# Kernel tuning notes

Hardware: AMD Instinct MI355X
Metric: run time of the kernel (lower is better)

## Reference

```python
import jax, jax.numpy as jnp
import numpy as np

N_NODES = 100000
N_EDGES = 1600000
N_GRAPHS = 1024
F = 128
L = 3  # num_gnn_layers
EPS = 1e-5


def _ln(x, g, b):
    mu = jnp.mean(x, axis=-1, keepdims=True)
    v = jnp.mean((x - mu) ** 2, axis=-1, keepdims=True)
    return (x - mu) * jax.lax.rsqrt(v + EPS) * g + b


def setup_inputs() -> dict:
    key = jax.random.key(0)
    ks = jax.random.split(key, 40)
    s = 0.05
    d = {}
    d['x'] = jax.random.normal(ks[0], (N_NODES, F), jnp.float32)
    d['w'] = jax.random.uniform(ks[1], (N_NODES, 1), jnp.float32)
    d['edge_index'] = jax.random.randint(ks[2], (2, N_EDGES), 0, N_NODES)
    d['batch'] = jnp.sort(jax.random.randint(ks[3], (N_NODES,), 0, N_GRAPHS))
    # input linear: (monomer_features+1) -> gc_features
    d['W_in'] = jax.random.normal(ks[4], (F + 1, F), jnp.float32) * s
    d['b_in'] = jnp.zeros((F,), jnp.float32)
    # stacked GCBlock params [L, ...]
    d['sage_Wl'] = jax.random.normal(ks[5], (L, F, F), jnp.float32) * s
    d['sage_bl'] = jnp.zeros((L, F), jnp.float32)
    d['sage_Wr'] = jax.random.normal(ks[6], (L, F, F), jnp.float32) * s
    d['ln1_g'] = jnp.ones((L, F), jnp.float32)
    d['ln1_b'] = jnp.zeros((L, F), jnp.float32)
    d['lin1_W'] = jax.random.normal(ks[7], (L, F, F), jnp.float32) * s
    d['lin1_b'] = jnp.zeros((L, F), jnp.float32)
    d['lin2_W'] = jax.random.normal(ks[8], (L, F, F), jnp.float32) * s
    d['lin2_b'] = jnp.zeros((L, F), jnp.float32)
    d['ln2_g'] = jnp.ones((L, F), jnp.float32)
    d['ln2_b'] = jnp.zeros((L, F), jnp.float32)
    # MeanDiffFeatureBlock: Linear(2F -> F)
    d['mdf_W'] = jax.random.normal(ks[9], (2 * F, F), jnp.float32) * s
    d['mdf_b'] = jnp.zeros((F,), jnp.float32)
    # mean PoolingLayer params
    d['pln1_g'] = jnp.ones((F,), jnp.float32)
    d['pln1_b'] = jnp.zeros((F,), jnp.float32)
    d['plin1_W'] = jax.random.normal(ks[10], (F, F), jnp.float32) * s
    d['plin1_b'] = jnp.zeros((F,), jnp.float32)
    d['plin2_W'] = jax.random.normal(ks[11], (F, F), jnp.float32) * s
    d['plin2_b'] = jnp.zeros((F,), jnp.float32)
    d['pln2_g'] = jnp.ones((F,), jnp.float32)
    d['pln2_b'] = jnp.zeros((F,), jnp.float32)
    return d


def reference(x, w, edge_index, batch, W_in, b_in, sage_Wl, sage_bl, sage_Wr,
              ln1_g, ln1_b, lin1_W, lin1_b, lin2_W, lin2_b, ln2_g, ln2_b,
              mdf_W, mdf_b, pln1_g, pln1_b, plin1_W, plin1_b, plin2_W, plin2_b,
              pln2_g, pln2_b):
    src, dst = edge_index[0], edge_index[1]
    # in-degree for SAGE mean aggregation (clamped so isolated nodes -> 0 agg)
    deg = jax.ops.segment_sum(jnp.ones((N_EDGES,), jnp.float32), dst,
                              num_segments=N_NODES)
    deg = jnp.maximum(deg, 1.0)[:, None]
    # graph sizes for global_mean_pool
    cnt = jax.ops.segment_sum(jnp.ones((N_NODES,), jnp.float32), batch,
                              num_segments=N_GRAPHS)
    cnt = jnp.maximum(cnt, 1.0)[:, None]

    # inilinear on [x, weight-fraction]  (scalers are identity at init)
    h = jnp.concatenate([x, w], axis=-1) @ W_in + b_in  # [N, F]

    def gc_block(h, p):
        Wl, bl, Wr, g1, b1, W1, bb1, W2, bb2, g2, b2 = p
        # SAGEConv: lin_l(mean_j x_j) + lin_r(x_i)
        agg = jax.ops.segment_sum(h[src], dst, num_segments=N_NODES) / deg
        y = agg @ Wl + bl + h @ Wr
        y1 = _ln(y + h, g1, b1)
        y2 = jax.nn.elu(y1 @ W1 + bb1) @ W2 + bb2  # dropout = identity (eval)
        return _ln(y2 + y1, g2, b2), None

    h, _ = jax.lax.scan(gc_block, h,
                        (sage_Wl, sage_bl, sage_Wr, ln1_g, ln1_b,
                         lin1_W, lin1_b, lin2_W, lin2_b, ln2_g, ln2_b))

    # MeanDiffFeatureBlock
    gm = jax.ops.segment_sum(h, batch, num_segments=N_GRAPHS) / cnt  # [B, F]
    h = jnp.concatenate([h, h - gm[batch]], axis=-1) @ mdf_W + mdf_b

    # mean PoolingLayer
    p = jax.ops.segment_sum(h, batch, num_segments=N_GRAPHS) / cnt  # [B, F]
    hh = _ln(p, pln1_g, pln1_b)
    y = jax.nn.elu(hh @ plin1_W + plin1_b) @ plin2_W + plin2_b
    return _ln(y + hh, pln2_g, pln2_b)  # [B, F]
```

## Files before the change

### kernel.cpp

```cpp
#include <hip/hip_runtime.h>
#include <math.h>

#define NN 100000
#define NE 1600000
#define NG 1024
#define FF 128
#define BSH 9
#define NBK ((NN + 511) >> BSH)
#define RB 512
#define BCAP 16384

typedef __attribute__((ext_vector_type(8))) short short8;
typedef __attribute__((ext_vector_type(4))) float f32x4;
typedef __attribute__((ext_vector_type(2))) float f32x2;

__device__ __forceinline__ unsigned short f2b(float f) {
    union { float f; unsigned u; } v; v.f = f;
    unsigned r = (v.u + 0x7FFF + ((v.u >> 16) & 1)) >> 16;
    return (unsigned short)r;
}
__device__ __forceinline__ float us2f(unsigned short u) {
    union { unsigned u; float f; } v; v.u = ((unsigned)u) << 16; return v.f;
}
__device__ __forceinline__ float fast_elu(float v) {
    float e = __builtin_amdgcn_exp2f(v * 1.44269504088896340736f) - 1.0f;
    return v > 0.f ? v : e;
}
__device__ __forceinline__ uint2 pk8(const float* v) {
    unsigned lo = 0, hi = 0;
    lo = (unsigned)__builtin_amdgcn_cvt_pk_fp8_f32(v[0], v[1], (int)lo, false);
    lo = (unsigned)__builtin_amdgcn_cvt_pk_fp8_f32(v[2], v[3], (int)lo, true);
    hi = (unsigned)__builtin_amdgcn_cvt_pk_fp8_f32(v[4], v[5], (int)hi, false);
    hi = (unsigned)__builtin_amdgcn_cvt_pk_fp8_f32(v[6], v[7], (int)hi, true);
    uint2 r; r.x = lo; r.y = hi; return r;
}
#define MFMA(a, b, c) __builtin_amdgcn_mfma_f32_16x16x32_bf16((a), (b), (c), 0, 0, 0)

__global__ __launch_bounds__(256)
void radix_scatter(const int* __restrict__ src, const int* __restrict__ dst,
                   int* __restrict__ bcur, unsigned* __restrict__ pairs, int n) {
    __shared__ int base[NBK];
    __shared__ int cnt[NBK];
    for (int i = threadIdx.x; i < NBK; i += 256) cnt[i] = 0;
    __syncthreads();
    const int per = (n + RB - 1) / RB;
    const int beg = blockIdx.x * per;
    const int end = min(n, beg + per);
    for (int i = beg + threadIdx.x; i < end; i += 256)
        atomicAdd(&cnt[dst[i] >> BSH], 1);
    __syncthreads();
    for (int i = threadIdx.x; i < NBK; i += 256)
        base[i] = cnt[i] ? atomicAdd(&bcur[i], cnt[i]) : 0;
    __syncthreads();
    for (int i = beg + threadIdx.x; i < end; i += 256) {
        int d = dst[i];
        int p = atomicAdd(&base[d >> BSH], 1);
        pairs[p] = ((unsigned)src[i] << BSH) | (unsigned)(d & 511);
    }
}

__global__ __launch_bounds__(512)
void bucket_build(const unsigned* __restrict__ pairs, const int* __restrict__ bcur,
                  int* __restrict__ row_beg, int* __restrict__ row_end,
                  float* __restrict__ inv_deg, int* __restrict__ ssrc) {
    __shared__ int cnt[512];
    __shared__ int curs[512];
    __shared__ int wsum[8];
    const int b = blockIdx.x;
    const int n0 = b << BSH;
    const int t = threadIdx.x;
    const int lane = t & 63, wid = t >> 6;

    cnt[t] = 0;
    __syncthreads();
    const int beg = b * BCAP, end = bcur[b];
    for (int i = beg + t; i < end; i += 512)
        atomicAdd(&cnt[pairs[i] & 511], 1);
    __syncthreads();

    int c = cnt[t];
    int x = c;
    #pragma unroll
    for (int o = 1; o < 64; o <<= 1) {
        int y = __shfl_up(x, o);
        if (lane >= o) x += y;
    }
    if (lane == 63) wsum[wid] = x;
    __syncthreads();
    if (t == 0) {
        int s = 0;
        #pragma unroll
        for (int w2 = 0; w2 < 8; ++w2) { int tv = wsum[w2]; wsum[w2] = s; s += tv; }
    }
    __syncthreads();
    int g0 = beg + wsum[wid] + x - c;
    curs[t] = g0;
    {
        int node = n0 + t;
        if (node < NN) {
            row_beg[node] = g0; row_end[node] = g0 + c;
            inv_deg[node] = 1.0f / (float)(c > 1 ? c : 1);
        }
    }
    __syncthreads();
    for (int i = beg + t; i < end; i += 512) {
        unsigned pr = pairs[i];
        int p = atomicAdd(&curs[pr & 511], 1);
        ssrc[p] = (int)(pr >> BSH) << 7;
    }
}

__global__ __launch_bounds__(256)
void graph_offsets(const int* __restrict__ batch, int* __restrict__ g_off,
                   float* __restrict__ inv_cnt, int* __restrict__ bcur,
                   int* __restrict__ ssrc) {
    int g = blockIdx.x * blockDim.x + threadIdx.x;
    if (g == 0) ssrc[0] = 0;
    if (g < NBK) bcur[g] = g * BCAP;
    if (g > NG) return;
    if (g == NG) { g_off[NG] = NN; return; }
    int lo = 0, hi = NN;
    while (lo < hi) { int mid = (lo + hi) >> 1; if (batch[mid] < g) lo = mid + 1; else hi = mid; }
    int lo2 = lo, hi2 = NN;
    while (lo2 < hi2) { int mid = (lo2 + hi2) >> 1; if (batch[mid] < g + 1) lo2 = mid + 1; else hi2 = mid; }
    g_off[g] = lo;
    int c = lo2 - lo;
    inv_cnt[g] = 1.0f / (float)(c > 1 ? c : 1);
}

struct WTab { const float* a[16]; };
__global__ __launch_bounds__(256)
void prep_weights(WTab tab, unsigned short* __restrict__ dst) {
    int w = blockIdx.x >> 6;
    int idx = ((blockIdx.x & 63) << 8) + threadIdx.x;
    int j = idx & 7, lane = (idx >> 3) & 63, nt = (idx >> 9) & 7, kc = idx >> 12;
    int cb = lane & 15, rq = lane >> 4;
    int k = kc * 32 + rq * 8 + j;
    int n = nt * 16 + cb;
    dst[(size_t)w * 16384 + idx] = f2b(tab.a[w][k * 128 + n]);
}

__global__ __launch_bounds__(256)
void sage_agg(const unsigned char* __restrict__ h8, const int* __restrict__ row_beg,
              const int* __restrict__ row_end, const float* __restrict__ inv_deg,
              const int* __restrict__ ssrc, unsigned short* __restrict__ aggb) {
    const int wid = threadIdx.x >> 6;
    const int lane = threadIdx.x & 63;
    const int n0 = blockIdx.x * 8 + wid * 2;
    const int n1 = n0 + 1;
    const int eg = lane >> 4, j = lane & 15;
    const int jo = j * 8;
    const int beg0 = row_beg[n0], end0 = row_end[n0];
    const int beg1 = row_beg[n1], end1 = row_end[n1];
    f32x2 a0 = {0.f, 0.f}, a1 = {0.f, 0.f}, a2 = {0.f, 0.f}, a3 = {0.f, 0.f};
    f32x2 b0 = {0.f, 0.f}, b1 = {0.f, 0.f}, b2 = {0.f, 0.f}, b3 = {0.f, 0.f};
    int e0 = beg0 + eg, e1 = beg1 + eg;
    const int d0 = end0 - beg0, d1 = end1 - beg1;
    const int nit = ((d0 > d1 ? d0 : d1) + 31) >> 5;
    for (int it = 0; it < nit; ++it, e0 += 32, e1 += 32) {
        uint2 u0[8], u1[8];
        #pragma unroll
        for (int k = 0; k < 8; ++k) {
            int ek = e0 + 4 * k;
            bool ok = ek < end0;
            int idx = ssrc[ok ? ek : 0];
            uint2 uu = *(const uint2*)(h8 + (unsigned)(idx + jo));
            uu.x = ok ? uu.x : 0u;
            uu.y = ok ? uu.y : 0u;
            u0[k] = uu;
        }
        #pragma unroll
        for (int k = 0; k < 8; ++k) {
            int ek = e1 + 4 * k;
            bool ok = ek < end1;
            int idx = ssrc[ok ? ek : 0];
            uint2 uu = *(const uint2*)(h8 + (unsigned)(idx + jo));
            uu.x = ok ? uu.x : 0u;
            uu.y = ok ? uu.y : 0u;
            u1[k] = uu;
        }
        #pragma unroll
        for (int k = 0; k < 8; ++k) {
            a0 += __builtin_amdgcn_cvt_pk_f32_fp8(u0[k].x, false);
            a1 += __builtin_amdgcn_cvt_pk_f32_fp8(u0[k].x, true);
            a2 += __builtin_amdgcn_cvt_pk_f32_fp8(u0[k].y, false);
            a3 += __builtin_amdgcn_cvt_pk_f32_fp8(u0[k].y, true);
            b0 += __builtin_amdgcn_cvt_pk_f32_fp8(u1[k].x, false);
            b1 += __builtin_amdgcn_cvt_pk_f32_fp8(u1[k].x, true);
            b2 += __builtin_amdgcn_cvt_pk_f32_fp8(u1[k].y, false);
            b3 += __builtin_amdgcn_cvt_pk_f32_fp8(u1[k].y, true);
        }
    }
    float af[8] = {a0.x, a0.y, a1.x, a1.y, a2.x, a2.y, a3.x, a3.y};
    float bf[8] = {b0.x, b0.y, b1.x, b1.y, b2.x, b2.y, b3.x, b3.y};
    #pragma unroll
    for (int k = 0; k < 8; ++k) {
        af[k] += __shfl_xor(af[k], 16);
        af[k] += __shfl_xor(af[k], 32);
        bf[k] += __shfl_xor(bf[k], 16);
        bf[k] += __shfl_xor(bf[k], 32);
    }
    if (eg == 0) {
        float id0 = inv_deg[n0];
        float id1 = inv_deg[n1];
        #pragma unroll
        for (int nt = 0; nt < 8; ++nt) {
            aggb[(size_t)n0 * 128 + nt * 16 + j] = f2b(af[nt] * id0);
            aggb[(size_t)n1 * 128 + nt * 16 + j] = f2b(bf[nt] * id1);
        }
    }
}

__global__ __launch_bounds__(256)
void pool_mean_b(const unsigned short* __restrict__ src, const int* __restrict__ g_off,
                 const float* __restrict__ inv_cnt, float* __restrict__ out) {
    __shared__ float red[3][128];
    const int g = blockIdx.x;
    const int t = threadIdx.x;
    const int lane = t & 63, wid = t >> 6;
    const int j = lane & 15, rs = lane >> 4;
    const int beg = g_off[g], end = g_off[g + 1];
    float s[8] = {0.f, 0.f, 0.f, 0.f, 0.f, 0.f, 0.f, 0.f};
    for (int n = beg + rs + wid * 4; n < end; n += 16) {
        short8 v = *(const short8*)&src[(size_t)n * FF + j * 8];
        #pragma unroll
        for (int i = 0; i < 8; ++i) s[i] += us2f((unsigned short)v[i]);
    }
    #pragma unroll
    for (int i = 0; i < 8; ++i) {
        s[i] += __shfl_xor(s[i], 16);
        s[i] += __shfl_xor(s[i], 32);
    }
    if (wid > 0 && rs == 0) {
        #pragma unroll
        for (int i = 0; i < 8; ++i) red[wid - 1][j * 8 + i] = s[i];
    }
    __syncthreads();
    if (wid == 0 && rs == 0) {
        float ic = inv_cnt[g];
        #pragma unroll
        for (int i = 0; i < 8; ++i) {
            float v = s[i] + red[0][j * 8 + i] + red[1][j * 8 + i] + red[2][j * 8 + i];
            out[(size_t)g * FF + j * 8 + i] = v * ic;
        }
    }
}

template<bool AB16, bool R1, int RESM, int ACT, bool LN, bool OF32, bool OB16, bool OB8>
__global__ __launch_bounds__(256)
void gemm_mfma(const void* __restrict__ A_,
               const unsigned short* __restrict__ Wf,
               const float* __restrict__ bias,
               const float* __restrict__ rvec, const float* __restrict__ rrow,
               const float* __restrict__ res,
               const float* __restrict__ lng, const float* __restrict__ lnb,
               float* __restrict__ outf, unsigned short* __restrict__ outb,
               unsigned char* __restrict__ outb8, int M) {
    __shared__ short Al[64 * 136];

    const int t = threadIdx.x;
    const int lane = t & 63, wid = t >> 6;
    const int m0 = blockIdx.x * 64;
    const int cb = lane & 15, rq = lane >> 4;
    const int band = wid * 16;

    if (AB16) {
        const unsigned short* Ab = (const unsigned short*)A_;
        #pragma unroll
        for (int i2 = 0; i2 < 4; ++i2) {
            int i = lane + i2 * 64;
            int row = band + (i >> 4), seg = i & 15;
            int gr = m0 + row; if (gr >= M) gr = M - 1;
            *(uint4*)&Al[row * 136 + seg * 8] = *(const uint4*)&Ab[(size_t)gr * 128 + seg * 8];
        }
    } else {
        const float* Af = (const float*)A_;
        #pragma unroll
        for (int i2 = 0; i2 < 8; ++i2) {
            int i = lane + i2 * 64;
            int row = band + (i >> 5), seg = i & 31;
            int gr = m0 + row; if (gr >= M) gr = M - 1;
            float4 v = *(const float4*)&Af[(size_t)gr * 128 + seg * 4];
            ushort4 o = {f2b(v.x), f2b(v.y), f2b(v.z), f2b(v.w)};
            *(ushort4*)&Al[row * 136 + seg * 4] = o;
        }
    }

    f32x4 acc[8];
    #pragma unroll
    for (int nt = 0; nt < 8; ++nt) acc[nt] = (f32x4){0.f, 0.f, 0.f, 0.f};

    const int aoff_base = (band + cb) * 136 + rq * 8;
    for (int kc = 0; kc < 4; ++kc) {
        short8 a0 = *(const short8*)&Al[aoff_base + kc * 32];
        #pragma unroll
        for (int nt = 0; nt < 8; ++nt) {
            short8 b0 = *(const short8*)&Wf[(size_t)(kc * 8 + nt) * 512 + lane * 8];
            acc[nt] = MFMA(a0, b0, acc[nt]);
        }
    }

    float bs[8], rr[8], lg[8], lb[8];
    #pragma unroll
    for (int nt = 0; nt < 8; ++nt) {
        int col = nt * 16 + cb;
        bs[nt] = bias[col];
        if (R1) rr[nt] = rrow[col];
        if (LN) { lg[nt] = lng[col]; lb[nt] = lnb[col]; }
    }
    #pragma unroll
    for (int reg = 0; reg < 4; ++reg) {
        int m = m0 + band + rq * 4 + reg;
        int mc = m < M ? m : M - 1;
        float v[8];
        #pragma unroll
        for (int nt = 0; nt < 8; ++nt) v[nt] = acc[nt][reg] + bs[nt];
        if (R1) {
            float rv = rvec[mc];
            #pragma unroll
            for (int nt = 0; nt < 8; ++nt) v[nt] += rv * rr[nt];
        }
        if (RESM == 1) {
            #pragma unroll
            for (int nt = 0; nt < 8; ++nt) v[nt] += res[(size_t)mc * 128 + nt * 16 + cb];
        }
        if (ACT == 1) {
            #pragma unroll
            for (int nt = 0; nt < 8; ++nt) v[nt] = fast_elu(v[nt]);
        }
        if (LN) {
            float s1 = 0.f, s2 = 0.f;
            #pragma unroll
            for (int nt = 0; nt < 8; ++nt) { s1 += v[nt]; s2 += v[nt] * v[nt]; }
            #pragma unroll
            for (int o = 8; o >= 1; o >>= 1) { s1 += __shfl_xor(s1, o); s2 += __shfl_xor(s2, o); }
            float mu = s1 * (1.f / 128.f);
            float rs = rsqrtf(s2 * (1.f / 128.f) - mu * mu + 1e-5f);
            #pragma unroll
            for (int nt = 0; nt < 8; ++nt) v[nt] = (v[nt] - mu) * rs * lg[nt] + lb[nt];
        }
        if (m < M) {
            #pragma unroll
            for (int nt = 0; nt < 8; ++nt) {
                size_t o = (size_t)m * 128 + nt * 16 + cb;
                if (OF32) outf[o] = v[nt];
                if (OB16) outb[o] = f2b(v[nt]);
            }
            if (OB8) *(uint2*)&outb8[(size_t)m * 128 + cb * 8] = pk8(v);
        }
    }
}

__global__ __launch_bounds__(256)
void gc_chain(const unsigned short* __restrict__ hin, const unsigned short* __restrict__ aggb,
              unsigned short* __restrict__ hout, unsigned char* __restrict__ h8out,
              const unsigned short* __restrict__ Wl_f, const unsigned short* __restrict__ Wr_f,
              const unsigned short* __restrict__ W1_f, const unsigned short* __restrict__ W2_f,
              const float* __restrict__ bl,
              const float* __restrict__ g1, const float* __restrict__ b1,
              const float* __restrict__ bb1, const float* __restrict__ bb2,
              const float* __restrict__ g2, const float* __restrict__ b2, int M) {
    __shared__ short Hl[64 * 136];
    __shared__ short Gl[64 * 136];

    const int t = threadIdx.x;
    const int lane = t & 63, wid = t >> 6;
    const int m0 = blockIdx.x * 64;
    const int cb = lane & 15, rq = lane >> 4;
    const int band = wid * 16;
    const int aoff_base = (band + cb) * 136 + rq * 8;
    const int boff = lane * 8;

    #pragma unroll
    for (int i2 = 0; i2 < 4; ++i2) {
        int i = lane + i2 * 64;
        int row = band + (i >> 4), seg = i & 15;
        int gr = m0 + row; if (gr >= M) gr = M - 1;
        *(uint4*)&Hl[row * 136 + seg * 8] = *(const uint4*)&hin[(size_t)gr * 128 + seg * 8];
        *(uint4*)&Gl[row * 136 + seg * 8] = *(const uint4*)&aggb[(size_t)gr * 128 + seg * 8];
    }

    f32x4 acc[8];
    #pragma unroll
    for (int nt = 0; nt < 8; ++nt) acc[nt] = (f32x4){0.f, 0.f, 0.f, 0.f};

    for (int kc = 0; kc < 4; ++kc) {
        short8 a0 = *(const short8*)&Gl[aoff_base + kc * 32];
        short8 a1 = *(const short8*)&Hl[aoff_base + kc * 32];
        #pragma unroll
        for (int nt = 0; nt < 8; ++nt) {
            const size_t wo = (size_t)(kc * 8 + nt) * 512 + boff;
            acc[nt] = MFMA(a0, *(const short8*)&Wl_f[wo], acc[nt]);
            acc[nt] = MFMA(a1, *(const short8*)&Wr_f[wo], acc[nt]);
        }
    }

    float y1r[4][8];
    {
        float bs[8], lg[8], lb[8];
        #pragma unroll
        for (int nt = 0; nt < 8; ++nt) {
            int col = nt * 16 + cb;
            bs[nt] = bl[col]; lg[nt] = g1[col]; lb[nt] = b1[col];
        }
        #pragma unroll
        for (int reg = 0; reg < 4; ++reg) {
            int r = band + rq * 4 + reg;
            float v[8];
            float s1 = 0.f, s2 = 0.f;
            #pragma unroll
            for (int nt = 0; nt < 8; ++nt) {
                v[nt] = acc[nt][reg] + bs[nt] + us2f((unsigned short)Hl[r * 136 + nt * 16 + cb]);
                s1 += v[nt]; s2 += v[nt] * v[nt];
            }
            #pragma unroll
            for (int o = 8; o >= 1; o >>= 1) { s1 += __shfl_xor(s1, o); s2 += __shfl_xor(s2, o); }
            float mu = s1 * (1.f / 128.f);
            float rs = rsqrtf(s2 * (1.f / 128.f) - mu * mu + 1e-5f);
            #pragma unroll
            for (int nt = 0; nt < 8; ++nt) {
                float y = (v[nt] - mu) * rs * lg[nt] + lb[nt];
                y1r[reg][nt] = y;
                Hl[r * 136 + nt * 16 + cb] = (short)f2b(y);
            }
        }
    }

    #pragma unroll
    for (int nt = 0; nt < 8; ++nt) acc[nt] = (f32x4){0.f, 0.f, 0.f, 0.f};
    for (int kc = 0; kc < 4; ++kc) {
        short8 a0 = *(const short8*)&Hl[aoff_base + kc * 32];
        #pragma unroll
        for (int nt = 0; nt < 8; ++nt)
            acc[nt] = MFMA(a0, *(const short8*)&W1_f[(size_t)(kc * 8 + nt) * 512 + boff], acc[nt]);
    }
    {
        float bs[8];
        #pragma unroll
        for (int nt = 0; nt < 8; ++nt) bs[nt] = bb1[nt * 16 + cb];
        #pragma unroll
        for (int reg = 0; reg < 4; ++reg) {
            int r = band + rq * 4 + reg;
            #pragma unroll
            for (int nt = 0; nt < 8; ++nt) {
                float v = fast_elu(acc[nt][reg] + bs[nt]);
                Gl[r * 136 + nt * 16 + cb] = (short)f2b(v);
            }
        }
    }

    #pragma unroll
    for (int nt = 0; nt < 8; ++nt) acc[nt] = (f32x4){0.f, 0.f, 0.f, 0.f};
    for (int kc = 0; kc < 4; ++kc) {
        short8 a0 = *(const short8*)&Gl[aoff_base + kc * 32];
        #pragma unroll
        for (int nt = 0; nt < 8; ++nt)
            acc[nt] = MFMA(a0, *(const short8*)&W2_f[(size_t)(kc * 8 + nt) * 512 + boff], acc[nt]);
    }
    {
        float bs[8], lg[8], lb[8];
        #pragma unroll
        for (int nt = 0; nt < 8; ++nt) {
            int col = nt * 16 + cb;
            bs[nt] = bb2[col]; lg[nt] = g2[col]; lb[nt] = b2[col];
        }
        #pragma unroll
        for (int reg = 0; reg < 4; ++reg) {
            int r = band + rq * 4 + reg;
            int m = m0 + r;
            float v[8];
            float s1 = 0.f, s2 = 0.f;
            #pragma unroll
            for (int nt = 0; nt < 8; ++nt) {
                v[nt] = acc[nt][reg] + bs[nt] + y1r[reg][nt];
                s1 += v[nt]; s2 += v[nt] * v[nt];
            }
            #pragma unroll
            for (int o = 8; o >= 1; o >>= 1) { s1 += __shfl_xor(s1, o); s2 += __shfl_xor(s2, o); }
            float mu = s1 * (1.f / 128.f);
            float rs = rsqrtf(s2 * (1.f / 128.f) - mu * mu + 1e-5f);
            if (m < M) {
                float fv[8];
                #pragma unroll
                for (int nt = 0; nt < 8; ++nt) {
                    fv[nt] = (v[nt] - mu) * rs * lg[nt] + lb[nt];
                    hout[(size_t)m * 128 + nt * 16 + cb] = f2b(fv[nt]);
                }
                *(uint2*)&h8out[(size_t)m * 128 + cb * 8] = pk8(fv);
            }
        }
    }
}

__global__ __launch_bounds__(256)
void head_chain(const float* __restrict__ gm,
                const unsigned short* __restrict__ Wa_f,
                const unsigned short* __restrict__ P1_f,
                const unsigned short* __restrict__ P2_f,
                const float* __restrict__ mdfb,
                const float* __restrict__ g1, const float* __restrict__ b1,
                const float* __restrict__ p1b, const float* __restrict__ p2b,
                const float* __restrict__ g2, const float* __restrict__ b2,
                float* __restrict__ outp) {
    __shared__ short Al[64 * 136];

    const int t = threadIdx.x;
    const int lane = t & 63, wid = t >> 6;
    const int m0 = blockIdx.x * 64;
    const int cb = lane & 15, rq = lane >> 4;
    const int band = wid * 16;
    const int aoff_base = (band + cb) * 136 + rq * 8;
    const int boff = lane * 8;

    #pragma unroll
    for (int i2 = 0; i2 < 8; ++i2) {
        int i = lane + i2 * 64;
        int row = band + (i >> 5), seg = i & 31;
        float4 v = *(const float4*)&gm[(size_t)(m0 + row) * 128 + seg * 4];
        ushort4 o = {f2b(v.x), f2b(v.y), f2b(v.z), f2b(v.w)};
        *(ushort4*)&Al[row * 136 + seg * 4] = o;
    }

    f32x4 acc[8];
    #pragma unroll
    for (int nt = 0; nt < 8; ++nt) acc[nt] = (f32x4){0.f, 0.f, 0.f, 0.f};
    for (int kc = 0; kc < 4; ++kc) {
        short8 a0 = *(const short8*)&Al[aoff_base + kc * 32];
        #pragma unroll
        for (int nt = 0; nt < 8; ++nt)
            acc[nt] = MFMA(a0, *(const short8*)&Wa_f[(size_t)(kc * 8 + nt) * 512 + boff], acc[nt]);
    }
    float y1r[4][8];
    {
        float bs[8], lg[8], lb[8];
        #pragma unroll
        for (int nt = 0; nt < 8; ++nt) {
            int col = nt * 16 + cb;
            bs[nt] = mdfb[col]; lg[nt] = g1[col]; lb[nt] = b1[col];
        }
        #pragma unroll
        for (int reg = 0; reg < 4; ++reg) {
            int r = band + rq * 4 + reg;
            float v[8];
            float s1 = 0.f, s2 = 0.f;
            #pragma unroll
            for (int nt = 0; nt < 8; ++nt) {
                v[nt] = acc[nt][reg] + bs[nt];
                s1 += v[nt]; s2 += v[nt] * v[nt];
            }
            #pragma unroll
            for (int o = 8; o >= 1; o >>= 1) { s1 += __shfl_xor(s1, o); s2 += __shfl_xor(s2, o); }
            float mu = s1 * (1.f / 128.f);
            float rs = rsqrtf(s2 * (1.f / 128.f) - mu * mu + 1e-5f);
            #pragma unroll
            for (int nt = 0; nt < 8; ++nt) {
                float y = (v[nt] - mu) * rs * lg[nt] + lb[nt];
                y1r[reg][nt] = y;
                Al[r * 136 + nt * 16 + cb] = (short)f2b(y);
            }
        }
    }

    #pragma unroll
    for (int nt = 0; nt < 8; ++nt) acc[nt] = (f32x4){0.f, 0.f, 0.f, 0.f};
    for (int kc = 0; kc < 4; ++kc) {
        short8 a0 = *(const short8*)&Al[aoff_base + kc * 32];
        #pragma unroll
        for (int nt = 0; nt < 8; ++nt)
            acc[nt] = MFMA(a0, *(const short8*)&P1_f[(size_t)(kc * 8 + nt) * 512 + boff], acc[nt]);
    }
    {
        float bs[8];
        #pragma unroll
        for (int nt = 0; nt < 8; ++nt) bs[nt] = p1b[nt * 16 + cb];
        #pragma unroll
        for (int reg = 0; reg < 4; ++reg) {
            int r = band + rq * 4 + reg;
            #pragma unroll
            for (int nt = 0; nt < 8; ++nt) {
                float v = fast_elu(acc[nt][reg] + bs[nt]);
                Al[r * 136 + nt * 16 + cb] = (short)f2b(v);
            }
        }
    }

    #pragma unroll
    for (int nt = 0; nt < 8; ++nt) acc[nt] = (f32x4){0.f, 0.f, 0.f, 0.f};
    for (int kc = 0; kc < 4; ++kc) {
        short8 a0 = *(const short8*)&Al[aoff_base + kc * 32];
        #pragma unroll
        for (int nt = 0; nt < 8; ++nt)
            acc[nt] = MFMA(a0, *(const short8*)&P2_f[(size_t)(kc * 8 + nt) * 512 + boff], acc[nt]);
    }
    {
        float bs[8], lg[8], lb[8];
        #pragma unroll
        for (int nt = 0; nt < 8; ++nt) {
            int col = nt * 16 + cb;
            bs[nt] = p2b[col]; lg[nt] = g2[col]; lb[nt] = b2[col];
        }
        #pragma unroll
        for (int reg = 0; reg < 4; ++reg) {
            int r = band + rq * 4 + reg;
            int m = m0 + r;
            float v[8];
            float s1 = 0.f, s2 = 0.f;
            #pragma unroll
            for (int nt = 0; nt < 8; ++nt) {
                v[nt] = acc[nt][reg] + bs[nt] + y1r[reg][nt];
                s1 += v[nt]; s2 += v[nt] * v[nt];
            }
            #pragma unroll
            for (int o = 8; o >= 1; o >>= 1) { s1 += __shfl_xor(s1, o); s2 += __shfl_xor(s2, o); }
            float mu = s1 * (1.f / 128.f);
            float rs = rsqrtf(s2 * (1.f / 128.f) - mu * mu + 1e-5f);
            #pragma unroll
            for (int nt = 0; nt < 8; ++nt)
                outp[(size_t)m * 128 + nt * 16 + cb] = (v[nt] - mu) * rs * lg[nt] + lb[nt];
        }
    }
}

extern "C" void kernel_launch(void* const* d_in, const int* in_sizes, int n_in,
                              void* d_out, int out_size, void* d_ws, size_t ws_size,
                              hipStream_t stream) {
    const float* x      = (const float*)d_in[0];
    const float* w      = (const float*)d_in[1];
    const int*   ei     = (const int*)d_in[2];
    const int*   batch  = (const int*)d_in[3];
    const float* W_in   = (const float*)d_in[4];
    const float* b_in   = (const float*)d_in[5];
    const float* sage_Wl = (const float*)d_in[6];
    const float* sage_bl = (const float*)d_in[7];
    const float* sage_Wr = (const float*)d_in[8];
    const float* ln1_g  = (const float*)d_in[9];
    const float* ln1_b  = (const float*)d_in[10];
    const float* lin1_W = (const float*)d_in[11];
    const float* lin1_b = (const float*)d_in[12];
    const float* lin2_W = (const float*)d_in[13];
    const float* lin2_b = (const float*)d_in[14];
    const float* ln2_g  = (const float*)d_in[15];
    const float* ln2_b  = (const float*)d_in[16];
    const float* mdf_W  = (const float*)d_in[17];
    const float* mdf_b  = (const float*)d_in[18];
    const float* pln1_g = (const float*)d_in[19];
    const float* pln1_b = (const float*)d_in[20];
    const float* plin1_W = (const float*)d_in[21];
    const float* plin1_b = (const float*)d_in[22];
    const float* plin2_W = (const float*)d_in[23];
    const float* plin2_b = (const float*)d_in[24];
    const float* pln2_g = (const float*)d_in[25];
    const float* pln2_b = (const float*)d_in[26];
    float* out = (float*)d_out;

    const int* e_src = ei;
    const int* e_dst = ei + NE;

    float* ws = (float*)d_ws;
    size_t off = 0;
    float* gm    = ws + off; off += (size_t)NG * FF;
    float* hh    = ws + off; off += (size_t)NG * FF;
    float* tt    = ws + off; off += (size_t)NG * FF;
    float* inv_deg = ws + off; off += NN;
    float* inv_cnt = ws + off; off += NG;
    unsigned short* us = (unsigned short*)(ws + off);
    size_t uoff = 0;
    unsigned short* hb0  = us + uoff; uoff += (size_t)NN * FF;
    unsigned short* hb1  = us + uoff; uoff += (size_t)NN * FF;
    unsigned short* aggb = us + uoff; uoff += (size_t)NN * FF;
    unsigned short* wt   = us + uoff; uoff += (size_t)16 * 16384;
    int* iw = (int*)(us + uoff);
    size_t ioff = 0;
    unsigned* pairs = (unsigned*)iw; ioff += (size_t)NBK * BCAP;
    int* ssrc    = iw + ioff; ioff += (size_t)NBK * BCAP;
    int* row_beg = iw + ioff; ioff += NN;
    int* row_end = iw + ioff; ioff += NN;
    int* g_off   = iw + ioff; ioff += NG + 1;
    int* bcur    = iw + ioff; ioff += NBK;
    unsigned char* h8 = (unsigned char*)pairs;

    WTab tab;
    tab.a[0] = W_in;
    for (int l = 0; l < 3; ++l) {
        tab.a[1 + l]  = sage_Wl + (size_t)l * 16384;
        tab.a[4 + l]  = sage_Wr + (size_t)l * 16384;
        tab.a[7 + l]  = lin1_W + (size_t)l * 16384;
        tab.a[10 + l] = lin2_W + (size_t)l * 16384;
    }
    tab.a[13] = mdf_W;
    tab.a[14] = plin1_W;
    tab.a[15] = plin2_W;
    prep_weights<<<16 * 64, 256, 0, stream>>>(tab, wt);
    const unsigned short* win_t = wt + 0 * 16384;
    const unsigned short* wa_t  = wt + 13 * 16384;
    const unsigned short* p1_t  = wt + 14 * 16384;
    const unsigned short* p2_t  = wt + 15 * 16384;

    graph_offsets<<<(NG + 256) / 256, 256, 0, stream>>>(batch, g_off, inv_cnt, bcur, ssrc);
    radix_scatter<<<RB, 256, 0, stream>>>(e_src, e_dst, bcur, pairs, NE);
    bucket_build<<<NBK, 512, 0, stream>>>(pairs, bcur, row_beg, row_end, inv_deg, ssrc);

    const int GN = (NN + 63) / 64;
    const int GB = NG / 64;

    gemm_mfma<false, true, 0, 0, false, false, true, true><<<GN, 256, 0, stream>>>(
        x, win_t, b_in, w, W_in + 128 * 128,
        nullptr, nullptr, nullptr, nullptr, hb0, h8, NN);

    unsigned short* hcur = hb0;
    unsigned short* hnxt = hb1;
    for (int l = 0; l < 3; ++l) {
        sage_agg<<<NN / 8, 256, 0, stream>>>(h8, row_beg, row_end, inv_deg, ssrc, aggb);
        gc_chain<<<GN, 256, 0, stream>>>(
            hcur, aggb, hnxt, h8,
            wt + (size_t)(1 + l) * 16384, wt + (size_t)(4 + l) * 16384,
            wt + (size_t)(7 + l) * 16384, wt + (size_t)(10 + l) * 16384,
            sage_bl + (size_t)l * FF,
            ln1_g + (size_t)l * FF, ln1_b + (size_t)l * FF,
            lin1_b + (size_t)l * FF, lin2_b + (size_t)l * FF,
            ln2_g + (size_t)l * FF, ln2_b + (size_t)l * FF, NN);
        unsigned short* tmp = hcur; hcur = hnxt; hnxt = tmp;
    }

    pool_mean_b<<<NG, 256, 0, stream>>>(hcur, g_off, inv_cnt, gm);
    head_chain<<<GB, 256, 0, stream>>>(
        gm, wa_t, p1_t, p2_t, mdf_b,
        pln1_g, pln1_b, plin1_b, plin2_b, pln2_g, pln2_b, out);
    (void)hh; (void)tt;
}
```

Before: 492.0 us.

## Fold graph_offsets into other kernels and vectorize edge bucketing loads

Removes the separate graph_offsets launch by moving bucket-cursor init into prep_weights and the per-graph binary searches into bucket_build. prep_weights now uses 16 blocks, each converting one whole weight matrix to bf16 in shared memory before permuting it, instead of 1024 small blocks. radix_scatter and bucket_build read dst, src and pairs as int4 or uint4 to cut load instructions. The intent is fewer launches and wider memory accesses. The price is that prep_weights now runs on only 16 blocks, and the per-graph binary searches delay the first few bucket_build blocks.

```diff
diff --git a/kernel.cpp b/kernel.cpp
--- a/kernel.cpp
+++ b/kernel.cpp
@@ -43,26 +43,53 @@
     __shared__ int cnt[NBK];
     for (int i = threadIdx.x; i < NBK; i += 256) cnt[i] = 0;
     __syncthreads();
-    const int per = (n + RB - 1) / RB;
+    const int per = (((n + RB - 1) / RB) + 3) & ~3;
     const int beg = blockIdx.x * per;
     const int end = min(n, beg + per);
-    for (int i = beg + threadIdx.x; i < end; i += 256)
-        atomicAdd(&cnt[dst[i] >> BSH], 1);
+    {
+        int i = beg + 4 * (int)threadIdx.x;
+        for (; i + 3 < end; i += 1024) {
+            int4 d4 = *(const int4*)&dst[i];
+            atomicAdd(&cnt[d4.x >> BSH], 1);
+            atomicAdd(&cnt[d4.y >> BSH], 1);
+            atomicAdd(&cnt[d4.z >> BSH], 1);
+            atomicAdd(&cnt[d4.w >> BSH], 1);
+        }
+        for (; i < end; ++i) atomicAdd(&cnt[dst[i] >> BSH], 1);
+    }
     __syncthreads();
     for (int i = threadIdx.x; i < NBK; i += 256)
         base[i] = cnt[i] ? atomicAdd(&bcur[i], cnt[i]) : 0;
     __syncthreads();
-    for (int i = beg + threadIdx.x; i < end; i += 256) {
-        int d = dst[i];
-        int p = atomicAdd(&base[d >> BSH], 1);
-        pairs[p] = ((unsigned)src[i] << BSH) | (unsigned)(d & 511);
+    {
+        int i = beg + 4 * (int)threadIdx.x;
+        for (; i + 3 < end; i += 1024) {
+            int4 d4 = *(const int4*)&dst[i];
+            int4 s4 = *(const int4*)&src[i];
+            int p;
+            p = atomicAdd(&base[d4.x >> BSH], 1);
+            pairs[p] = ((unsigned)s4.x << BSH) | (unsigned)(d4.x & 511);
+            p = atomicAdd(&base[d4.y >> BSH], 1);
+            pairs[p] = ((unsigned)s4.y << BSH) | (unsigned)(d4.y & 511);
+            p = atomicAdd(&base[d4.z >> BSH], 1);
+            pairs[p] = ((unsigned)s4.z << BSH) | (unsigned)(d4.z & 511);
+            p = atomicAdd(&base[d4.w >> BSH], 1);
+            pairs[p] = ((unsigned)s4.w << BSH) | (unsigned)(d4.w & 511);
+        }
+        for (; i < end; ++i) {
+            int d = dst[i];
+            int p = atomicAdd(&base[d >> BSH], 1);
+            pairs[p] = ((unsigned)src[i] << BSH) | (unsigned)(d & 511);
+        }
     }
 }
 
 __global__ __launch_bounds__(512)
 void bucket_build(const unsigned* __restrict__ pairs, const int* __restrict__ bcur,
                   int* __restrict__ row_beg, int* __restrict__ row_end,
-                  float* __restrict__ inv_deg, int* __restrict__ ssrc) {
+                  float* __restrict__ inv_deg, int* __restrict__ ssrc,
+                  const int* __restrict__ batch, int* __restrict__ g_off,
+                  float* __restrict__ inv_cnt) {
     __shared__ int cnt[512];
     __shared__ int curs[512];
     __shared__ int wsum[8];
@@ -71,11 +98,37 @@
     const int t = threadIdx.x;
     const int lane = t & 63, wid = t >> 6;
 
+    {
+        int g = b * 512 + t;
+        if (g <= NG) {
+            if (g == NG) {
+                g_off[NG] = NN;
+            } else {
+                int lo = 0, hi = NN;
+                while (lo < hi) { int mid = (lo + hi) >> 1; if (batch[mid] < g) lo = mid + 1; else hi = mid; }
+                int lo2 = lo, hi2 = NN;
+                while (lo2 < hi2) { int mid = (lo2 + hi2) >> 1; if (batch[mid] < g + 1) lo2 = mid + 1; else hi2 = mid; }
+                g_off[g] = lo;
+                int c = lo2 - lo;
+                inv_cnt[g] = 1.0f / (float)(c > 1 ? c : 1);
+            }
+        }
+    }
+
     cnt[t] = 0;
     __syncthreads();
     const int beg = b * BCAP, end = bcur[b];
-    for (int i = beg + t; i < end; i += 512)
-        atomicAdd(&cnt[pairs[i] & 511], 1);
+    {
+        int i = beg + 4 * t;
+        for (; i + 3 < end; i += 2048) {
+            uint4 p4 = *(const uint4*)&pairs[i];
+            atomicAdd(&cnt[p4.x & 511], 1);
+            atomicAdd(&cnt[p4.y & 511], 1);
+            atomicAdd(&cnt[p4.z & 511], 1);
+            atomicAdd(&cnt[p4.w & 511], 1);
+        }
+        for (; i < end; ++i) atomicAdd(&cnt[pairs[i] & 511], 1);
+    }
     __syncthreads();
 
     int c = cnt[t];
@@ -103,41 +156,51 @@
         }
     }
     __syncthreads();
-    for (int i = beg + t; i < end; i += 512) {
-        unsigned pr = pairs[i];
-        int p = atomicAdd(&curs[pr & 511], 1);
-        ssrc[p] = (int)(pr >> BSH) << 7;
-    }
-}
-
-__global__ __launch_bounds__(256)
-void graph_offsets(const int* __restrict__ batch, int* __restrict__ g_off,
-                   float* __restrict__ inv_cnt, int* __restrict__ bcur,
-                   int* __restrict__ ssrc) {
-    int g = blockIdx.x * blockDim.x + threadIdx.x;
-    if (g == 0) ssrc[0] = 0;
-    if (g < NBK) bcur[g] = g * BCAP;
-    if (g > NG) return;
-    if (g == NG) { g_off[NG] = NN; return; }
-    int lo = 0, hi = NN;
-    while (lo < hi) { int mid = (lo + hi) >> 1; if (batch[mid] < g) lo = mid + 1; else hi = mid; }
-    int lo2 = lo, hi2 = NN;
-    while (lo2 < hi2) { int mid = (lo2 + hi2) >> 1; if (batch[mid] < g + 1) lo2 = mid + 1; else hi2 = mid; }
-    g_off[g] = lo;
-    int c = lo2 - lo;
-    inv_cnt[g] = 1.0f / (float)(c > 1 ? c : 1);
+    {
+        int i = beg + 4 * t;
+        for (; i + 3 < end; i += 2048) {
+            uint4 p4 = *(const uint4*)&pairs[i];
+            int p;
+            p = atomicAdd(&curs[p4.x & 511], 1); ssrc[p] = (int)(p4.x >> BSH) << 7;
+            p = atomicAdd(&curs[p4.y & 511], 1); ssrc[p] = (int)(p4.y >> BSH) << 7;
+            p = atomicAdd(&curs[p4.z & 511], 1); ssrc[p] = (int)(p4.z >> BSH) << 7;
+            p = atomicAdd(&curs[p4.w & 511], 1); ssrc[p] = (int)(p4.w >> BSH) << 7;
+        }
+        for (; i < end; ++i) {
+            unsigned pr = pairs[i];
+            int p = atomicAdd(&curs[pr & 511], 1);
+            ssrc[p] = (int)(pr >> BSH) << 7;
+        }
+    }
 }
 
 struct WTab { const float* a[16]; };
 __global__ __launch_bounds__(256)
-void prep_weights(WTab tab, unsigned short* __restrict__ dst) {
-    int w = blockIdx.x >> 6;
-    int idx = ((blockIdx.x & 63) << 8) + threadIdx.x;
-    int j = idx & 7, lane = (idx >> 3) & 63, nt = (idx >> 9) & 7, kc = idx >> 12;
-    int cb = lane & 15, rq = lane >> 4;
-    int k = kc * 32 + rq * 8 + j;
-    int n = nt * 16 + cb;
-    dst[(size_t)w * 16384 + idx] = f2b(tab.a[w][k * 128 + n]);
+void prep_weights(WTab tab, unsigned short* __restrict__ dst,
+                  int* __restrict__ bcur, int* __restrict__ ssrc) {
+    __shared__ unsigned short Wl[128 * 128];
+    const int w = blockIdx.x;
+    const int t = threadIdx.x;
+    if (w == 0) {
+        for (int i = t; i < NBK; i += 256) bcur[i] = i * BCAP;
+        if (t == 0) ssrc[0] = 0;
+    }
+    const float4* src = (const float4*)tab.a[w];
+    for (int i = t; i < 4096; i += 256) {
+        float4 v = src[i];
+        ushort4 o = {f2b(v.x), f2b(v.y), f2b(v.z), f2b(v.w)};
+        *(ushort4*)&Wl[i * 4] = o;
+    }
+    __syncthreads();
+    unsigned short* dw = dst + (size_t)w * 16384;
+    for (int i2 = 0; i2 < 64; ++i2) {
+        int idx = t + i2 * 256;
+        int j = idx & 7, lane = (idx >> 3) & 63, nt = (idx >> 9) & 7, kc = idx >> 12;
+        int cb = lane & 15, rq = lane >> 4;
+        int k = kc * 32 + rq * 8 + j;
+        int n = nt * 16 + cb;
+        dw[idx] = Wl[k * 128 + n];
+    }
 }
 
 __global__ __launch_bounds__(256)
@@ -690,15 +753,15 @@
     tab.a[13] = mdf_W;
     tab.a[14] = plin1_W;
     tab.a[15] = plin2_W;
-    prep_weights<<<16 * 64, 256, 0, stream>>>(tab, wt);
+    prep_weights<<<16, 256, 0, stream>>>(tab, wt, bcur, ssrc);
     const unsigned short* win_t = wt + 0 * 16384;
     const unsigned short* wa_t  = wt + 13 * 16384;
     const unsigned short* p1_t  = wt + 14 * 16384;
     const unsigned short* p2_t  = wt + 15 * 16384;
 
-    graph_offsets<<<(NG + 256) / 256, 256, 0, stream>>>(batch, g_off, inv_cnt, bcur, ssrc);
     radix_scatter<<<RB, 256, 0, stream>>>(e_src, e_dst, bcur, pairs, NE);
-    bucket_build<<<NBK, 512, 0, stream>>>(pairs, bcur, row_beg, row_end, inv_deg, ssrc);
+    bucket_build<<<NBK, 512, 0, stream>>>(pairs, bcur, row_beg, row_end,
+                                          inv_deg, ssrc, batch, g_off, inv_cnt);
 
     const int GN = (NN + 63) / 64;
     const int GB = NG / 64;
```

New measurement: 489.4 us. Within noise of the previous version (-0.5%).
